# Kernel tuning notes

Measured on AMD Instinct MI355X. Metric: run time of the kernel, lower is better.

## Reference

```python
import jax, jax.numpy as jnp
import numpy as np
import math

D_MODEL = 1024
N_HEADS = 16
D_K = D_MODEL // N_HEADS
B, T = 4, 2048


def setup_inputs() -> dict:
    key = jax.random.key(0)
    ks = jax.random.split(key, 5)
    s = 1.0 / math.sqrt(D_MODEL)
    return {
        "x": jax.random.normal(ks[0], (B, T, D_MODEL), dtype=jnp.float32),
        "W_qkv": jax.random.normal(ks[1], (3 * D_MODEL, D_MODEL), dtype=jnp.float32) * s,
        "b_qkv": jax.random.normal(ks[2], (3 * D_MODEL,), dtype=jnp.float32) * 0.01,
        "W_out": jax.random.normal(ks[3], (D_MODEL, D_MODEL), dtype=jnp.float32) * s,
        "b_out": jax.random.normal(ks[4], (D_MODEL,), dtype=jnp.float32) * 0.01,
    }


def reference(x, W_qkv, b_qkv, W_out, b_out):
    Bn, Tn, C = x.shape
    # qkv projection: [B,T,3C]
    qkv = jnp.einsum("btc,oc->bto", x, W_qkv) + b_qkv
    # NOTE: original reshapes to (B,T,H,3*d_k) THEN chunks -> per-head interleaved layout
    qkv = qkv.reshape(Bn, Tn, N_HEADS, 3 * D_K).transpose(0, 2, 1, 3)  # [B,H,T,3dk]
    q, k, v = jnp.split(qkv, 3, axis=-1)  # each [B,H,T,dk]
    scores = jnp.einsum("bhtd,bhsd->bhts", q, k) / math.sqrt(D_K)
    causal = jnp.tril(jnp.ones((Tn, Tn), dtype=bool))
    scores = jnp.where(causal[None, None], scores, -jnp.inf)
    attn = jax.nn.softmax(scores, axis=-1)
    ctx = jnp.einsum("bhts,bhsd->bhtd", attn, v)  # [B,H,T,dk]
    ctx = ctx.transpose(0, 2, 1, 3).reshape(Bn, Tn, C)
    return jnp.einsum("btc,oc->bto", ctx, W_out) + b_out
```

## Files before the change

kernel.cpp:

```cpp
#include <hip/hip_runtime.h>

typedef __attribute__((ext_vector_type(8))) short short8;
typedef __attribute__((ext_vector_type(4))) float f32x4;
typedef __attribute__((ext_vector_type(16))) float f32x16;
typedef __attribute__((ext_vector_type(4))) unsigned int u32x4;
typedef __attribute__((ext_vector_type(4))) unsigned short u16x4;
typedef unsigned int u32;
typedef unsigned short u16;

#define DEV static __device__ __forceinline__

DEV u16 f2bf(float f) {
  union { float f; u32 u; } c; c.f = f;
  u32 r = (c.u + 0x7fffu + ((c.u >> 16) & 1u)) >> 16;
  return (u16)r;
}
DEV float bf2f(u16 v) {
  union { u32 u; float f; } c; c.u = ((u32)v) << 16;
  return c.f;
}
DEV short8 pack8(float4 a, float4 b) {
  short8 r;
  r[0]=(short)f2bf(a.x); r[1]=(short)f2bf(a.y); r[2]=(short)f2bf(a.z); r[3]=(short)f2bf(a.w);
  r[4]=(short)f2bf(b.x); r[5]=(short)f2bf(b.y); r[6]=(short)f2bf(b.z); r[7]=(short)f2bf(b.w);
  return r;
}
DEV u32 cvtpk(float lo, float hi) {
  u32 r;
  asm("v_cvt_pk_bf16_f32 %0, %1, %2" : "=v"(r) : "v"(lo), "v"(hi));
  return r;
}

#if __has_builtin(__builtin_amdgcn_exp2f)
DEV float fexp2(float x) { return __builtin_amdgcn_exp2f(x); }
#else
DEV float fexp2(float x) { return exp2f(x); }
#endif

DEV void glds16(const void* g, void* l) {
  __builtin_amdgcn_global_load_lds((const __attribute__((address_space(1))) u32*)g,
                                   (__attribute__((address_space(3))) u32*)l, 16, 0, 0);
}

DEV f32x16 mfma32(short8 a, short8 b, f32x16 c) {
  return __builtin_amdgcn_mfma_f32_32x32x16_bf16(a, b, c, 0, 0, 0);
}

constexpr int CDIM = 1024, TT = 2048, NH = 16, DK = 64;
#define QSC 0.1803368801111601f

__global__ void conv_bf16(const float* __restrict__ X, const float* __restrict__ W1,
                          const float* __restrict__ W2, u16* __restrict__ Xb,
                          u16* __restrict__ W1b, u16* __restrict__ W2b) {
  const long n0 = 1048576, n1 = 393216, n2 = 131072;
  for (long i = (long)blockIdx.x * blockDim.x + threadIdx.x; i < n0 + n1 + n2;
       i += (long)gridDim.x * blockDim.x) {
    const float* s; u16* d; long j = i;
    if (j < n0) { s = X; d = Xb; }
    else if (j < n0 + n1) { j -= n0; s = W1; d = W1b; }
    else { j -= n0 + n1; s = W2; d = W2b; }
    float4 a = ((const float4*)s)[2 * j];
    float4 b = ((const float4*)s)[2 * j + 1];
    ((short8*)d)[j] = pack8(a, b);
  }
}

__global__ void __launch_bounds__(512, 2)
qkv_gemm4(const u16* __restrict__ A, const u16* __restrict__ B,
          const float* __restrict__ bias, u16* __restrict__ Qb,
          u16* __restrict__ Kb, u16* __restrict__ VTb) {
  __shared__ u16 LS[3][3][128][64];
  const int tid = threadIdx.x, lane = tid & 63, wid = tid >> 6;
  const int lo = lane & 15, lg = lane >> 4;
  const int wm = wid >> 1, wn = wid & 1;
  const int rin = lane >> 3, blk = lane & 7;
  const int m0 = blockIdx.x * 256, n0 = blockIdx.y * 128;
  const int r7 = lo & 7;

  const u16* gA = A + (size_t)(m0 + wid * 16 + rin) * CDIM + (blk ^ rin) * 8;
  const u16* gB = B + (size_t)(n0 + wid * 16 + rin) * CDIM + (blk ^ rin) * 8;
  u16* lsb = &LS[0][0][wid * 16][0];

#define STG3(bufi, kt)                                           \
  {                                                              \
    const int k0e = (kt) * 64;                                   \
    u16* lb = lsb + (bufi) * 24576;                              \
    glds16(gA + k0e, lb);                                        \
    glds16(gA + k0e + 8 * CDIM, lb + 512);                       \
    glds16(gA + k0e + 128 * CDIM, lb + 8192);                    \
    glds16(gA + k0e + 136 * CDIM, lb + 8704);                    \
    glds16(gB + k0e, lb + 16384);                                \
    glds16(gB + k0e + 8 * CDIM, lb + 16896);                     \
  }

  f32x4 acc[4][4];
  const f32x4 fz = {0.f, 0.f, 0.f, 0.f};
#pragma unroll
  for (int i = 0; i < 4; ++i)
#pragma unroll
    for (int j = 0; j < 4; ++j) acc[i][j] = fz;

  STG3(0, 0);
  STG3(1, 1);
  int b0 = 0, b1 = 1, b2 = 2;
  for (int T = 0; T < 16; ++T) {
    if (T < 14) {
      STG3(b2, T + 2);
      asm volatile("s_waitcnt vmcnt(12)" ::: "memory");
    } else if (T == 14) {
      asm volatile("s_waitcnt vmcnt(6)" ::: "memory");
    } else {
      asm volatile("s_waitcnt vmcnt(0)" ::: "memory");
    }
    __builtin_amdgcn_s_barrier();
    {
      const u16* pA = &LS[b0][wm >> 1][(wm & 1) * 64][0];
      const u16* pB = &LS[b0][2][wn * 64][0];
      short8 af[4][2], bfr[4][2];
#pragma unroll
      for (int mi = 0; mi < 4; ++mi)
#pragma unroll
        for (int kk = 0; kk < 2; ++kk)
          af[mi][kk] = *(const short8*)&pA[(mi * 16 + lo) * 64 + (((kk * 4 + lg) ^ r7) * 8)];
#pragma unroll
      for (int ni = 0; ni < 4; ++ni)
#pragma unroll
        for (int kk = 0; kk < 2; ++kk)
          bfr[ni][kk] = *(const short8*)&pB[(ni * 16 + lo) * 64 + (((kk * 4 + lg) ^ r7) * 8)];
      __builtin_amdgcn_s_setprio(1);
#pragma unroll
      for (int kk = 0; kk < 2; ++kk)
#pragma unroll
        for (int mi = 0; mi < 4; ++mi)
#pragma unroll
          for (int ni = 0; ni < 4; ++ni)
            acc[mi][ni] = __builtin_amdgcn_mfma_f32_16x16x32_bf16(af[mi][kk], bfr[ni][kk], acc[mi][ni], 0, 0, 0);
      __builtin_amdgcn_s_setprio(0);
    }
    __builtin_amdgcn_s_barrier();
    const int tmp = b0; b0 = b1; b1 = b2; b2 = tmp;
  }
#undef STG3

#pragma unroll
  for (int ni = 0; ni < 4; ++ni) {
    const int o = n0 + wn * 64 + ni * 16 + lo;
    const float bv = bias[o];
    const int hh = o / 192, rem = o - hh * 192, which = rem >> 6, d = rem & 63;
#pragma unroll
    for (int mi = 0; mi < 4; ++mi) {
      const int mb = m0 + wm * 64 + mi * 16 + lg * 4;
      const int bbi = mb >> 11, t0 = mb & 2047;
      const int bh = bbi * NH + hh;
      if (which == 2) {
        u16x4 pk;
#pragma unroll
        for (int r = 0; r < 4; ++r) pk[r] = f2bf(acc[mi][ni][r] + bv);
        *(u16x4*)&VTb[((size_t)bh * DK + d) * TT + t0] = pk;
      } else if (which == 1) {
#pragma unroll
        for (int r = 0; r < 4; ++r)
          Kb[((size_t)bh * TT + t0 + r) * DK + d] = f2bf(acc[mi][ni][r] + bv);
      } else {
#pragma unroll
        for (int r = 0; r < 4; ++r)
          Qb[((size_t)bh * TT + t0 + r) * DK + d] = f2bf((acc[mi][ni][r] + bv) * QSC);
      }
    }
  }
}

__global__ void __launch_bounds__(256, 4)
attn10(const u16* __restrict__ Qb, const u16* __restrict__ Kb,
       const u16* __restrict__ VTb, u16* __restrict__ PA, u16* __restrict__ PB,
       float* __restrict__ ML) {
  __shared__ u16 Kls[2][64][64];
  __shared__ u16 Vls[2][64][64];
  const int tid = threadIdx.x, lane = tid & 63, wv = tid >> 6;
  const int lq = lane & 31, h = lane >> 5;
  const int id = blockIdx.x;
  const int w = (id & 7) * 128 + (id >> 3);
  const int bh = w >> 4;
  const int pj = w & 7;
  const int sp = (w >> 3) & 1;
  const int bb = bh >> 4, head = bh & 15;
  const u16* Qp = Qb + (size_t)bh * TT * DK;
  const u16* Kp = Kb + (size_t)bh * TT * DK;
  const u16* Vp = VTb + (size_t)bh * DK * TT;
  const int rin = lane >> 3, blk = lane & 7;
  u16* PO = sp ? PB : PA;

  const u16* kga = Kp + (size_t)(wv * 16 + rin) * DK + (blk ^ rin) * 8;
  const u16* vga = Vp + (size_t)(wv * 16 + rin) * TT + (blk ^ rin) * 8;
  u16* kls0 = &Kls[0][wv * 16][0];
  u16* vls0 = &Vls[0][wv * 16][0];
  const int lds_half = 64 * 64;

#define STAGE10(bufi, kvt_)                                                 \
  {                                                                         \
    const int o_ = (bufi) * lds_half;                                       \
    glds16(kga + (size_t)(kvt_) * 4096, kls0 + o_);                         \
    glds16(kga + (size_t)(kvt_) * 4096 + 512, kls0 + o_ + 512);             \
    glds16(vga + (size_t)(kvt_) * 64, vls0 + o_);                           \
    glds16(vga + (size_t)(kvt_) * 64 + 8 * TT, vls0 + o_ + 512);            \
  }

  for (int pi = 0; pi < 2; ++pi) {
    const int qtile = pi ? (15 - pj) : pj;
    const int q0w = qtile * 128 + wv * 32;
    const int qrow = q0w + lq;

    short8 qw[4];
#pragma unroll
    for (int kk = 0; kk < 4; ++kk)
      qw[kk] = *(const short8*)&Qp[(size_t)qrow * DK + kk * 16 + h * 8];

    f32x16 oa0, oa1;
#pragma unroll
    for (int r = 0; r < 16; ++r) { oa0[r] = 0.f; oa1[r] = 0.f; }
    float l_s = 0.f;

    const int nt = 2 * qtile + 2;
    STAGE10(0, sp);
    __syncthreads();
    int buf = 0;
    for (int kvt = sp; kvt < nt; kvt += 2) {
      const int kv0 = kvt * 64;
      if (kvt + 2 < nt) STAGE10(buf ^ 1, kvt + 2);
      if (kv0 <= q0w + 31) {
        f32x16 s0, s1;
#pragma unroll
        for (int r = 0; r < 16; ++r) { s0[r] = 0.f; s1[r] = 0.f; }
        __builtin_amdgcn_s_setprio(1);
#pragma unroll
        for (int kk = 0; kk < 4; ++kk) {
          const short8 kf0 = *(const short8*)&Kls[buf][lq][(((2 * kk + h) ^ (lq & 7)) * 8)];
          const short8 kf1 = *(const short8*)&Kls[buf][32 + lq][(((2 * kk + h) ^ (lq & 7)) * 8)];
          s0 = mfma32(kf0, qw[kk], s0);
          s1 = mfma32(kf1, qw[kk], s1);
        }
        __builtin_amdgcn_s_setprio(0);
        const bool diag = (kv0 + 63 > q0w);
        if (diag) {
          const int lim = qrow - kv0 - 4 * h;
#pragma unroll
          for (int r = 0; r < 16; ++r) {
            const int kl = (r & 3) + 8 * (r >> 2);
            s0[r] = (kl <= lim) ? s0[r] : -1e30f;
            s1[r] = (kl + 32 <= lim) ? s1[r] : -1e30f;
          }
        }
        float rsa = 0.f, rsb = 0.f, rsc = 0.f, rsd = 0.f;
#pragma unroll
        for (int r = 0; r < 16; r += 4) {
          const float a0 = fexp2(s0[r]),     a1 = fexp2(s1[r]);
          const float b0 = fexp2(s0[r + 1]), b1 = fexp2(s1[r + 1]);
          const float c0 = fexp2(s0[r + 2]), c1 = fexp2(s1[r + 2]);
          const float d0 = fexp2(s0[r + 3]), d1 = fexp2(s1[r + 3]);
          s0[r] = a0; s1[r] = a1; s0[r + 1] = b0; s1[r + 1] = b1;
          s0[r + 2] = c0; s1[r + 2] = c1; s0[r + 3] = d0; s1[r + 3] = d1;
          rsa += a0 + a1; rsb += b0 + b1; rsc += c0 + c1; rsd += d0 + d1;
        }
        float rs = (rsa + rsb) + (rsc + rsd);
        rs += __shfl_xor(rs, 32);
        l_s += rs;
#pragma unroll
        for (int s = 0; s < 2; ++s) {
          u32 C[8];
#pragma unroll
          for (int j = 0; j < 8; ++j)
            C[j] = s ? cvtpk(s1[2 * j], s1[2 * j + 1]) : cvtpk(s0[2 * j], s0[2 * j + 1]);
#pragma unroll
          for (int b = 0; b < 2; ++b) {
            const int o = 4 * b;
            const u32 D1 = h ? C[o + 0] : C[o + 2];
            const u32 D2 = h ? C[o + 1] : C[o + 3];
            const u32 R1 = __shfl_xor(D1, 32);
            const u32 R2 = __shfl_xor(D2, 32);
            union { u32x4 w; short8 s8; } pa;
            pa.w[0] = h ? R1 : C[o + 0];
            pa.w[1] = h ? R2 : C[o + 1];
            pa.w[2] = h ? C[o + 2] : R1;
            pa.w[3] = h ? C[o + 3] : R2;
            const int ks = 2 * s + b;
            const short8 vb0 = *(const short8*)&Vls[buf][lq][(((2 * ks + h) ^ (lq & 7)) * 8)];
            const short8 vb1 = *(const short8*)&Vls[buf][32 + lq][(((2 * ks + h) ^ (lq & 7)) * 8)];
            __builtin_amdgcn_s_setprio(1);
            oa0 = mfma32(pa.s8, vb0, oa0);
            oa1 = mfma32(pa.s8, vb1, oa1);
            __builtin_amdgcn_s_setprio(0);
          }
        }
      }
      __syncthreads();
      buf ^= 1;
    }

#pragma unroll
    for (int r = 0; r < 16; ++r) {
      const int t = q0w + (r & 3) + 8 * (r >> 2) + 4 * h;
      const size_t rowb = ((size_t)(bb * TT + t)) * CDIM + head * DK;
      PO[rowb + lq] = f2bf(oa0[r]);
      PO[rowb + 32 + lq] = f2bf(oa1[r]);
    }
    if (h == 0) ML[((size_t)(sp * 64 + bh) << 11) + qrow] = l_s;
    __syncthreads();
  }
#undef STAGE10
}

__global__ void attn_merge(const u16* PA, const u16* PB,
                           const float* __restrict__ ML, u16* Ctx) {
  const int row = blockIdx.x;
  const int b = row >> 11, t = row & 2047;
  const int c = threadIdx.x * 4;
  const int head = c >> 6;
  const int bh = b * NH + head;
  const float lA = ML[((size_t)bh << 11) + t];
  const float lB = ML[((size_t)(64 + bh) << 11) + t];
  const float il = 1.0f / (lA + lB);
  const size_t idx = ((size_t)row) * CDIM + c;
  u16x4 pa = *(const u16x4*)&PA[idx];
  u16x4 pb = *(const u16x4*)&PB[idx];
  u16x4 o;
#pragma unroll
  for (int e = 0; e < 4; ++e) o[e] = f2bf((bf2f(pa[e]) + bf2f(pb[e])) * il);
  *(u16x4*)&Ctx[idx] = o;
}

__global__ void out_gemm2(const u16* __restrict__ A, const u16* __restrict__ B,
                          const float* __restrict__ bias, float* __restrict__ Out) {
  __shared__ u16 As[128][64];
  __shared__ u16 Bs[128][64];
  const int tid = threadIdx.x, lane = tid & 63, wv = tid >> 6;
  const int wr = wv >> 1, wc = wv & 1, lo = lane & 15, lg = lane >> 4;
  const int m0 = blockIdx.x * 128, n0 = blockIdx.y * 128;
  const int rin = lane >> 3, blk = lane & 7;

  f32x4 acc[4][4];
  const f32x4 fz = {0.f, 0.f, 0.f, 0.f};
#pragma unroll
  for (int i = 0; i < 4; ++i)
#pragma unroll
    for (int j = 0; j < 4; ++j) acc[i][j] = fz;

  for (int k0 = 0; k0 < CDIM; k0 += 64) {
    const u16* ga = A + (size_t)(m0 + 32 * wv + rin) * CDIM + k0 + blk * 8;
    const u16* gb = B + (size_t)(n0 + 32 * wv + rin) * CDIM + k0 + blk * 8;
#pragma unroll
    for (int i = 0; i < 4; ++i) glds16(ga + (size_t)(8 * i) * CDIM, &As[32 * wv + 8 * i][0]);
#pragma unroll
    for (int i = 0; i < 4; ++i) glds16(gb + (size_t)(8 * i) * CDIM, &Bs[32 * wv + 8 * i][0]);
    __syncthreads();
#pragma unroll
    for (int kk = 0; kk < 2; ++kk) {
      short8 af[4], bf[4];
#pragma unroll
      for (int mi = 0; mi < 4; ++mi) af[mi] = *(const short8*)&As[wr * 64 + mi * 16 + lo][kk * 32 + lg * 8];
#pragma unroll
      for (int ni = 0; ni < 4; ++ni) bf[ni] = *(const short8*)&Bs[wc * 64 + ni * 16 + lo][kk * 32 + lg * 8];
#pragma unroll
      for (int mi = 0; mi < 4; ++mi)
#pragma unroll
        for (int ni = 0; ni < 4; ++ni)
          acc[mi][ni] = __builtin_amdgcn_mfma_f32_16x16x32_bf16(af[mi], bf[ni], acc[mi][ni], 0, 0, 0);
    }
    __syncthreads();
  }

#pragma unroll
  for (int ni = 0; ni < 4; ++ni) {
    const int o = n0 + wc * 64 + ni * 16 + lo;
    const float bv = bias[o];
#pragma unroll
    for (int mi = 0; mi < 4; ++mi)
#pragma unroll
      for (int r = 0; r < 4; ++r)
        Out[(size_t)(m0 + wr * 64 + mi * 16 + lg * 4 + r) * CDIM + o] = acc[mi][ni][r] + bv;
  }
}

extern "C" void kernel_launch(void* const* d_in, const int* in_sizes, int n_in,
                              void* d_out, int out_size, void* d_ws, size_t ws_size,
                              hipStream_t stream) {
  const float* X = (const float*)d_in[0];
  const float* Wqkv = (const float*)d_in[1];
  const float* bqkv = (const float*)d_in[2];
  const float* Wout = (const float*)d_in[3];
  const float* bout = (const float*)d_in[4];
  float* Out = (float*)d_out;

  u16* Xb  = (u16*)d_ws;
  u16* W1b = Xb + 8388608;
  u16* W2b = W1b + 3145728;
  u16* Qb  = W2b + 1048576;
  u16* Kb  = Qb + 8388608;
  u16* VTb = Kb + 8388608;
  u16* Ctx = VTb + 8388608;

  conv_bf16<<<1024, 256, 0, stream>>>(X, Wqkv, Wout, Xb, W1b, W2b);
  qkv_gemm4<<<dim3(32, 24), 512, 0, stream>>>(Xb, W1b, bqkv, Qb, Kb, VTb);
  attn10<<<dim3(1024), 256, 0, stream>>>(Qb, Kb, VTb, Ctx, Xb, (float*)W1b);
  attn_merge<<<8192, 256, 0, stream>>>(Ctx, Xb, (const float*)W1b, Ctx);
  out_gemm2<<<dim3(64, 8), 256, 0, stream>>>(Ctx, W2b, bout, Out);
}
```

Baseline: 166.3 us.

## Split QKV GEMM k-tile into two half-phases interleaving LDS reads, loads and MFMA

Restructures the QKV projection GEMM main loop so each 64-wide k-tile is processed in two halves. Each half issues its LDS fragment reads and half of the next-next tile's global-to-LDS loads before its 16 MFMAs, with explicit barriers and sched_barriers. The aim is to overlap memory issue with matrix compute and to reduce register pressure from holding both k-halves of fragments at once. In exchange it adds more barriers per iteration and tighter waitcnt bookkeeping, which raises the risk of stalls or ordering mistakes.

```diff
diff --git a/kernel.cpp b/kernel.cpp
--- a/kernel.cpp
+++ b/kernel.cpp
@@ -66,7 +66,7 @@
 }
 
 __global__ void __launch_bounds__(512, 2)
-qkv_gemm4(const u16* __restrict__ A, const u16* __restrict__ B,
+qkv_gemm5(const u16* __restrict__ A, const u16* __restrict__ B,
           const float* __restrict__ bias, u16* __restrict__ Qb,
           u16* __restrict__ Kb, u16* __restrict__ VTb) {
   __shared__ u16 LS[3][3][128][64];
@@ -81,15 +81,20 @@
   const u16* gB = B + (size_t)(n0 + wid * 16 + rin) * CDIM + (blk ^ rin) * 8;
   u16* lsb = &LS[0][0][wid * 16][0];
 
-#define STG3(bufi, kt)                                           \
+#define STGH0(bufi, kt)                                          \
   {                                                              \
     const int k0e = (kt) * 64;                                   \
     u16* lb = lsb + (bufi) * 24576;                              \
     glds16(gA + k0e, lb);                                        \
     glds16(gA + k0e + 8 * CDIM, lb + 512);                       \
+    glds16(gB + k0e, lb + 16384);                                \
+  }
+#define STGH1(bufi, kt)                                          \
+  {                                                              \
+    const int k0e = (kt) * 64;                                   \
+    u16* lb = lsb + (bufi) * 24576;                              \
     glds16(gA + k0e + 128 * CDIM, lb + 8192);                    \
     glds16(gA + k0e + 136 * CDIM, lb + 8704);                    \
-    glds16(gB + k0e, lb + 16384);                                \
     glds16(gB + k0e + 8 * CDIM, lb + 16896);                     \
   }
 
@@ -100,47 +105,65 @@
 #pragma unroll
     for (int j = 0; j < 4; ++j) acc[i][j] = fz;
 
-  STG3(0, 0);
-  STG3(1, 1);
+  STGH0(0, 0); STGH1(0, 0);
+  STGH0(1, 1); STGH1(1, 1);
+  asm volatile("s_waitcnt vmcnt(6)" ::: "memory");
+  __builtin_amdgcn_s_barrier();
+
   int b0 = 0, b1 = 1, b2 = 2;
   for (int T = 0; T < 16; ++T) {
+    const u16* pA = &LS[b0][wm >> 1][(wm & 1) * 64][0];
+    const u16* pB = &LS[b0][2][wn * 64][0];
+    short8 af[4], bfr[4];
+#pragma unroll
+    for (int mi = 0; mi < 4; ++mi)
+      af[mi] = *(const short8*)&pA[(mi * 16 + lo) * 64 + ((lg ^ r7) * 8)];
+#pragma unroll
+    for (int ni = 0; ni < 4; ++ni)
+      bfr[ni] = *(const short8*)&pB[(ni * 16 + lo) * 64 + ((lg ^ r7) * 8)];
+    if (T < 14) STGH0(b2, T + 2);
+    __builtin_amdgcn_sched_barrier(0);
+    __builtin_amdgcn_s_barrier();
+    asm volatile("s_waitcnt lgkmcnt(0)" ::: "memory");
+    __builtin_amdgcn_sched_barrier(0);
+    __builtin_amdgcn_s_setprio(1);
+#pragma unroll
+    for (int mi = 0; mi < 4; ++mi)
+#pragma unroll
+      for (int ni = 0; ni < 4; ++ni)
+        acc[mi][ni] = __builtin_amdgcn_mfma_f32_16x16x32_bf16(af[mi], bfr[ni], acc[mi][ni], 0, 0, 0);
+    __builtin_amdgcn_s_setprio(0);
+    __builtin_amdgcn_sched_barrier(0);
+    __builtin_amdgcn_s_barrier();
+#pragma unroll
+    for (int mi = 0; mi < 4; ++mi)
+      af[mi] = *(const short8*)&pA[(mi * 16 + lo) * 64 + (((4 + lg) ^ r7) * 8)];
+#pragma unroll
+    for (int ni = 0; ni < 4; ++ni)
+      bfr[ni] = *(const short8*)&pB[(ni * 16 + lo) * 64 + (((4 + lg) ^ r7) * 8)];
+    if (T < 14) STGH1(b2, T + 2);
+    __builtin_amdgcn_sched_barrier(0);
     if (T < 14) {
-      STG3(b2, T + 2);
-      asm volatile("s_waitcnt vmcnt(12)" ::: "memory");
+      asm volatile("s_waitcnt vmcnt(6)" ::: "memory");
     } else if (T == 14) {
-      asm volatile("s_waitcnt vmcnt(6)" ::: "memory");
-    } else {
       asm volatile("s_waitcnt vmcnt(0)" ::: "memory");
     }
     __builtin_amdgcn_s_barrier();
-    {
-      const u16* pA = &LS[b0][wm >> 1][(wm & 1) * 64][0];
-      const u16* pB = &LS[b0][2][wn * 64][0];
-      short8 af[4][2], bfr[4][2];
-#pragma unroll
-      for (int mi = 0; mi < 4; ++mi)
-#pragma unroll
-        for (int kk = 0; kk < 2; ++kk)
-          af[mi][kk] = *(const short8*)&pA[(mi * 16 + lo) * 64 + (((kk * 4 + lg) ^ r7) * 8)];
+    asm volatile("s_waitcnt lgkmcnt(0)" ::: "memory");
+    __builtin_amdgcn_sched_barrier(0);
+    __builtin_amdgcn_s_setprio(1);
+#pragma unroll
+    for (int mi = 0; mi < 4; ++mi)
 #pragma unroll
       for (int ni = 0; ni < 4; ++ni)
-#pragma unroll
-        for (int kk = 0; kk < 2; ++kk)
-          bfr[ni][kk] = *(const short8*)&pB[(ni * 16 + lo) * 64 + (((kk * 4 + lg) ^ r7) * 8)];
-      __builtin_amdgcn_s_setprio(1);
-#pragma unroll
-      for (int kk = 0; kk < 2; ++kk)
-#pragma unroll
-        for (int mi = 0; mi < 4; ++mi)
-#pragma unroll
-          for (int ni = 0; ni < 4; ++ni)
-            acc[mi][ni] = __builtin_amdgcn_mfma_f32_16x16x32_bf16(af[mi][kk], bfr[ni][kk], acc[mi][ni], 0, 0, 0);
-      __builtin_amdgcn_s_setprio(0);
-    }
+        acc[mi][ni] = __builtin_amdgcn_mfma_f32_16x16x32_bf16(af[mi], bfr[ni], acc[mi][ni], 0, 0, 0);
+    __builtin_amdgcn_s_setprio(0);
+    __builtin_amdgcn_sched_barrier(0);
     __builtin_amdgcn_s_barrier();
     const int tmp = b0; b0 = b1; b1 = b2; b2 = tmp;
   }
-#undef STG3
+#undef STGH0
+#undef STGH1
 
 #pragma unroll
   for (int ni = 0; ni < 4; ++ni) {
@@ -399,7 +422,7 @@
   u16* Ctx = VTb + 8388608;
 
   conv_bf16<<<1024, 256, 0, stream>>>(X, Wqkv, Wout, Xb, W1b, W2b);
-  qkv_gemm4<<<dim3(32, 24), 512, 0, stream>>>(Xb, W1b, bqkv, Qb, Kb, VTb);
+  qkv_gemm5<<<dim3(32, 24), 512, 0, stream>>>(Xb, W1b, bqkv, Qb, Kb, VTb);
   attn10<<<dim3(1024), 256, 0, stream>>>(Qb, Kb, VTb, Ctx, Xb, (float*)W1b);
   attn_merge<<<8192, 256, 0, stream>>>(Ctx, Xb, (const float*)W1b, Ctx);
   out_gemm2<<<dim3(64, 8), 256, 0, stream>>>(Ctx, W2b, bout, Out);
```

New measurement: 163.0 us. 1.02x faster.
